# Performance work log

Hardware: AMD Instinct MI355X
Metric: run time of the kernel (lower is better)

## Reference

```python
import jax, jax.numpy as jnp
import numpy as np

ROWS, COLS = 1024, 1024
N_NODES = ROWS * COLS
RHO_W = 1000.0      # water density
RHO_I = 917.0       # ice density (unused in output path, kept for fidelity)
GRAV = 9.81
SEC_PER_A = 31556926.0
FLOW_COEFF = 0.0405
FLOW_EXP = 1.25     # 5/4
N_ITERS = 32        # fixed-point iterations for MFD flow accumulation


def _raster_links(rows, cols):
    ids = np.arange(rows * cols, dtype=np.int32).reshape(rows, cols)
    src_h = ids[:, :-1].ravel(); dst_h = ids[:, 1:].ravel()
    src_v = ids[:-1, :].ravel(); dst_v = ids[1:, :].ravel()
    return (np.concatenate([src_h, src_v]), np.concatenate([dst_h, dst_v]))


def setup_inputs() -> dict:
    key = jax.random.key(0)
    k1, k2, k3, k4 = jax.random.split(key, 4)
    melt_rate = jax.random.uniform(k1, (N_NODES,), jnp.float32) * 10.0          # m/a
    bedrock_elevation = jax.random.normal(k2, (N_NODES,), jnp.float32) * 500.0  # m
    water_pressure = jax.random.uniform(k3, (N_NODES,), jnp.float32) * 1.0e6    # Pa
    cell_area = jnp.full((N_NODES,), 1.0e4, jnp.float32)                        # 100m cells
    conduit_size = jax.random.uniform(k4, (N_NODES,), jnp.float32) + 0.01
    # landlab-style status: 0 = core node, 1 = fixed-value boundary (perimeter)
    status = np.zeros((ROWS, COLS), dtype=np.int32)
    status[0, :] = 1; status[-1, :] = 1; status[:, 0] = 1; status[:, -1] = 1
    src, dst = _raster_links(ROWS, COLS)
    return {
        "melt_rate": melt_rate,
        "bedrock_elevation": bedrock_elevation,
        "water_pressure": water_pressure,
        "cell_area": cell_area,
        "conduit_size": conduit_size,
        "status_at_node": jnp.asarray(status.ravel()),
        "link_src": jnp.asarray(src),
        "link_dst": jnp.asarray(dst),
    }


def reference(melt_rate, bedrock_elevation, water_pressure, cell_area,
              conduit_size, status_at_node, link_src, link_dst):
    n = melt_rate.shape[0]
    seg = lambda d, i: jax.ops.segment_sum(d, i, num_segments=n)

    # hydraulic potential (surface FlowDirectorMFD routes on)
    phi = RHO_W * GRAV * bedrock_elevation + water_pressure
    # local runoff input at each node
    runoff = melt_rate * cell_area / SEC_PER_A

    # MFD: split each node's outflow among downslope neighbors, proportional
    # to the positive potential drop along each link (unit link length).
    core = (status_at_node == 0)
    dphi = phi[link_src] - phi[link_dst]
    drop_fwd = jnp.maximum(dphi, 0.0) * core[link_src]   # src -> dst
    drop_bwd = jnp.maximum(-dphi, 0.0) * core[link_dst]  # dst -> src
    total_drop = seg(drop_fwd, link_src) + seg(drop_bwd, link_dst)
    s_safe = jnp.where(total_drop > 0.0, total_drop, 1.0)
    frac_fwd = drop_fwd / s_safe[link_src]
    frac_bwd = drop_bwd / s_safe[link_dst]

    # flow accumulation on the drainage DAG: Q = runoff + P^T Q (fixed-point)
    def step(q, _):
        inflow = seg(frac_fwd * q[link_src], link_dst) + seg(frac_bwd * q[link_dst], link_src)
        return runoff + inflow, None

    discharge, _ = jax.lax.scan(step, runoff, None, length=N_ITERS)

    # calc_hydraulic_gradient, masked to core nodes (status == 0)
    gradient = (discharge * FLOW_COEFF * conduit_size ** FLOW_EXP) ** 2
    return jnp.where(status_at_node == 0, gradient, 0.0)
```

## Files before the change

kernel.cpp:

```cpp
#include <hip/hip_runtime.h>

#define ROWS 1024
#define COLS 1024
#define NN (ROWS*COLS)

#define TILE_H 32
#define TILE_W 64
#define HALO   8
#define RH     48
#define RW     80
#define RC     (RH*RW)
#define SPR    (RW/4)
#define NSTRIP (RC/4)
#define NT     256
#define BR     (RH/4)
#define BC     (RW/4)
#define NB4    (BR*BC)

static constexpr float RHOG    = 1000.0f * 9.81f;
static constexpr float INV_SEC = 1.0f / 31556926.0f;
static constexpr float FLOWC   = 0.0405f;

__device__ __forceinline__ float4 gld4(const float* __restrict__ p, int g, bool in) {
    if (in) return *reinterpret_cast<const float4*>(p + g);
    return make_float4(0.f, 0.f, 0.f, 0.f);
}

__global__ __launch_bounds__(256) void k_pre(
        const float* __restrict__ bed, const float* __restrict__ pw,
        const int* __restrict__ status,
        const float* __restrict__ melt, const float* __restrict__ area,
        float* __restrict__ phi, float* __restrict__ inv,
        float* __restrict__ runoff) {
    int i = blockIdx.x * 256 + threadIdx.x;
    int r = i >> 10, c = i & (COLS - 1);
    float p = RHOG * bed[i] + pw[i];
    float t = 0.f;
    if (c > 0)        t += fmaxf(p - (RHOG * bed[i - 1]    + pw[i - 1]),    0.f);
    if (c < COLS - 1) t += fmaxf(p - (RHOG * bed[i + 1]    + pw[i + 1]),    0.f);
    if (r > 0)        t += fmaxf(p - (RHOG * bed[i - COLS] + pw[i - COLS]), 0.f);
    if (r < ROWS - 1) t += fmaxf(p - (RHOG * bed[i + COLS] + pw[i + COLS]), 0.f);
    phi[i]    = p;
    inv[i]    = (status[i] == 0 && t > 0.f) ? (1.f / t) : 0.f;
    runoff[i] = melt[i] * area[i] * INV_SEC;
}

template <bool FIRST, bool FINAL>
__global__ __launch_bounds__(256) void k_fused(
        const float* __restrict__ phi_g, const float* __restrict__ inv_g,
        const float* __restrict__ run_g, const float* __restrict__ qin,
        float* __restrict__ qout,
        const float* __restrict__ cond, const int* __restrict__ status) {
    __shared__ float A[RC];
    __shared__ float Bv[RC];
    __shared__ float4 plT[2][NB4], plB[2][NB4];
    __shared__ float4 plL[2][NB4], plR[2][NB4];
    const int tid = threadIdx.x;
    const int r0 = (int)blockIdx.y * TILE_H - HALO;
    const int c0 = (int)blockIdx.x * TILE_W - HALO;

#pragma unroll
    for (int k = 0; k < 4; ++k) {
        int sidx = tid + k * NT;
        if (sidx < NSTRIP) {
            int sr = sidx / SPR, sc4 = (sidx - sr * SPR) * 4;
            int gr = r0 + sr, gc = c0 + sc4;
            bool in = (gr >= 0) & (gr < ROWS) & (gc >= 0) & (gc < COLS);
            int g = gr * COLS + gc;
            *reinterpret_cast<float4*>(&A[sr * RW + sc4])  = gld4(phi_g, g, in);
            *reinterpret_cast<float4*>(&Bv[sr * RW + sc4]) = gld4(inv_g, g, in);
        }
    }
    __syncthreads();

    const bool active = (tid < NB4);
    const int br = tid / BC, bc = tid - (tid / BC) * BC;
    const int rr0 = 4 * br, cc0 = 4 * bc;
    const bool inter = (br >= 2) & (br <= BR - 3) & (bc >= 2) & (bc <= BC - 3);

    float wW[4][4], wE[4][4], wN[4][4], wS[4][4];
    float q[4][4], ro[4][4];
    int dd[4][4];

    if (active) {
#pragma unroll
        for (int i = 0; i < 4; ++i) {
            int rr = rr0 + i;
            int x = rr * RW + cc0;
            float4 pc = *reinterpret_cast<const float4*>(&A[x]);
            float4 ic = *reinterpret_cast<const float4*>(&Bv[x]);
            int xu = (rr > 0)      ? x - RW : x;
            int xd = (rr < RH - 1) ? x + RW : x;
            float4 pu = *reinterpret_cast<const float4*>(&A[xu]);
            float4 iu = *reinterpret_cast<const float4*>(&Bv[xu]);
            float4 pd = *reinterpret_cast<const float4*>(&A[xd]);
            float4 id = *reinterpret_cast<const float4*>(&Bv[xd]);
            float pl = (cc0 > 0)      ? A[x - 1]  : pc.x;
            float il = (cc0 > 0)      ? Bv[x - 1] : 0.f;
            float pr = (cc0 < RW - 4) ? A[x + 4]  : pc.w;
            float ir = (cc0 < RW - 4) ? Bv[x + 4] : 0.f;
            wN[i][0] = fmaxf(pu.x - pc.x, 0.f) * iu.x;
            wN[i][1] = fmaxf(pu.y - pc.y, 0.f) * iu.y;
            wN[i][2] = fmaxf(pu.z - pc.z, 0.f) * iu.z;
            wN[i][3] = fmaxf(pu.w - pc.w, 0.f) * iu.w;
            wS[i][0] = fmaxf(pd.x - pc.x, 0.f) * id.x;
            wS[i][1] = fmaxf(pd.y - pc.y, 0.f) * id.y;
            wS[i][2] = fmaxf(pd.z - pc.z, 0.f) * id.z;
            wS[i][3] = fmaxf(pd.w - pc.w, 0.f) * id.w;
            wW[i][0] = fmaxf(pl   - pc.x, 0.f) * il;
            wW[i][1] = fmaxf(pc.x - pc.y, 0.f) * ic.x;
            wW[i][2] = fmaxf(pc.y - pc.z, 0.f) * ic.y;
            wW[i][3] = fmaxf(pc.z - pc.w, 0.f) * ic.z;
            wE[i][0] = fmaxf(pc.y - pc.x, 0.f) * ic.y;
            wE[i][1] = fmaxf(pc.z - pc.y, 0.f) * ic.z;
            wE[i][2] = fmaxf(pc.w - pc.z, 0.f) * ic.w;
            wE[i][3] = fmaxf(pr   - pc.w, 0.f) * ir;
        }
#pragma unroll
        for (int i = 0; i < 4; ++i)
#pragma unroll
            for (int j = 0; j < 4; ++j) {
                int rr = rr0 + i, cc = cc0 + j;
                dd[i][j] = min(min(rr, RH - 1 - rr), min(cc, RW - 1 - cc));
            }
#pragma unroll
        for (int i = 0; i < 4; ++i) {
            int gr = r0 + rr0 + i, gc = c0 + cc0;
            bool in = (gr >= 0) & (gr < ROWS) & (gc >= 0) & (gc < COLS);
            int g = gr * COLS + gc;
            float4 r4 = gld4(run_g, g, in);
            ro[i][0] = r4.x; ro[i][1] = r4.y; ro[i][2] = r4.z; ro[i][3] = r4.w;
            float4 q4 = FIRST ? r4 : gld4(qin, g, in);
            q[i][0] = q4.x; q[i][1] = q4.y; q[i][2] = q4.z; q[i][3] = q4.w;
        }
        plT[0][tid] = make_float4(q[0][0], q[0][1], q[0][2], q[0][3]);
        plB[0][tid] = make_float4(q[3][0], q[3][1], q[3][2], q[3][3]);
        plL[0][tid] = make_float4(q[0][0], q[1][0], q[2][0], q[3][0]);
        plR[0][tid] = make_float4(q[0][3], q[1][3], q[2][3], q[3][3]);
    }
    __syncthreads();

    for (int s = 0; s < HALO; ++s) {
        const int pp = s & 1, pn = pp ^ 1;
        if (active) {
            float4 up = plB[pp][(br > 0)      ? tid - BC : tid];
            float4 dn = plT[pp][(br < BR - 1) ? tid + BC : tid];
            float4 lf = plR[pp][(bc > 0)      ? tid - 1  : tid];
            float4 rt = plL[pp][(bc < BC - 1) ? tid + 1  : tid];
            float upv[4] = {up.x, up.y, up.z, up.w};
            float dnv[4] = {dn.x, dn.y, dn.z, dn.w};
            float lfv[4] = {lf.x, lf.y, lf.z, lf.w};
            float rtv[4] = {rt.x, rt.y, rt.z, rt.w};
            float nq[4][4];
#pragma unroll
            for (int i = 0; i < 4; ++i)
#pragma unroll
                for (int j = 0; j < 4; ++j) {
                    float uv = (i > 0) ? q[i - 1][j] : upv[j];
                    float dv = (i < 3) ? q[i + 1][j] : dnv[j];
                    float lv = (j > 0) ? q[i][j - 1] : lfv[i];
                    float rv = (j < 3) ? q[i][j + 1] : rtv[i];
                    float a = ro[i][j];
                    a = fmaf(wW[i][j], lv, a);
                    a = fmaf(wE[i][j], rv, a);
                    a = fmaf(wN[i][j], uv, a);
                    a = fmaf(wS[i][j], dv, a);
                    nq[i][j] = a;
                }
            if (!inter) {
#pragma unroll
                for (int i = 0; i < 4; ++i)
#pragma unroll
                    for (int j = 0; j < 4; ++j)
                        nq[i][j] = (s < dd[i][j]) ? nq[i][j] : q[i][j];
            }
#pragma unroll
            for (int i = 0; i < 4; ++i)
#pragma unroll
                for (int j = 0; j < 4; ++j) q[i][j] = nq[i][j];
            plT[pn][tid] = make_float4(q[0][0], q[0][1], q[0][2], q[0][3]);
            plB[pn][tid] = make_float4(q[3][0], q[3][1], q[3][2], q[3][3]);
            plL[pn][tid] = make_float4(q[0][0], q[1][0], q[2][0], q[3][0]);
            plR[pn][tid] = make_float4(q[0][3], q[1][3], q[2][3], q[3][3]);
        }
        __syncthreads();
    }

    if (active && inter) {
#pragma unroll
        for (int i = 0; i < 4; ++i) {
            int g = (r0 + rr0 + i) * COLS + (c0 + cc0);
            if (FINAL) {
                float4 c4 = *reinterpret_cast<const float4*>(cond + g);
                int4 st   = *reinterpret_cast<const int4*>(status + g);
                float4 o;
                float t;
                t = q[i][0] * FLOWC * (c4.x * sqrtf(sqrtf(c4.x))); o.x = (st.x == 0) ? t * t : 0.f;
                t = q[i][1] * FLOWC * (c4.y * sqrtf(sqrtf(c4.y))); o.y = (st.y == 0) ? t * t : 0.f;
                t = q[i][2] * FLOWC * (c4.z * sqrtf(sqrtf(c4.z))); o.z = (st.z == 0) ? t * t : 0.f;
                t = q[i][3] * FLOWC * (c4.w * sqrtf(sqrtf(c4.w))); o.w = (st.w == 0) ? t * t : 0.f;
                *reinterpret_cast<float4*>(qout + g) = o;
            } else {
                *reinterpret_cast<float4*>(qout + g) =
                    make_float4(q[i][0], q[i][1], q[i][2], q[i][3]);
            }
        }
    }
}

extern "C" void kernel_launch(void* const* d_in, const int* in_sizes, int n_in,
                              void* d_out, int out_size, void* d_ws, size_t ws_size,
                              hipStream_t stream) {
    const float* melt   = (const float*)d_in[0];
    const float* bed    = (const float*)d_in[1];
    const float* pw     = (const float*)d_in[2];
    const float* area   = (const float*)d_in[3];
    const float* cond   = (const float*)d_in[4];
    const int*   status = (const int*)d_in[5];
    float* out = (float*)d_out;

    char* ws = (char*)d_ws;
    float* phi    = (float*)(ws);
    float* inv    = (float*)(ws + 4ull  * NN);
    float* runoff = (float*)(ws + 8ull  * NN);
    float* qA     = (float*)(ws + 12ull * NN);
    float* qB     = (float*)(ws + 16ull * NN);

    k_pre<<<dim3(NN / 256), dim3(256), 0, stream>>>(bed, pw, status, melt, area,
                                                    phi, inv, runoff);

    dim3 grid(COLS / TILE_W, ROWS / TILE_H), block(NT);
    k_fused<true,  false><<<grid, block, 0, stream>>>(phi, inv, runoff, runoff, qA, nullptr, nullptr);
    k_fused<false, false><<<grid, block, 0, stream>>>(phi, inv, runoff, qA, qB, nullptr, nullptr);
    k_fused<false, false><<<grid, block, 0, stream>>>(phi, inv, runoff, qB, qA, nullptr, nullptr);
    k_fused<false, true ><<<grid, block, 0, stream>>>(phi, inv, runoff, qA, out, cond, status);
}
```

Baseline: 141.8 us.

## Fuse preprocessing into stencil kernel and double halo to halve launches

Removes the separate preprocessing kernel: each tile now recomputes phi, the inverse total drop and runoff from raw inputs in shared memory, including a one-cell apron. The halo grows from 8 to 16, so 32 iterations take two fused launches instead of four, and the workspace arrays for phi, inv and runoff go away. In exchange each tile does more redundant halo work (a 64x96 region for a 32x64 output) with 384 threads, and the ping-pong planes reuse the phi LDS buffer after a barrier.

```diff
diff --git a/kernel.cpp b/kernel.cpp
--- a/kernel.cpp
+++ b/kernel.cpp
@@ -6,16 +6,21 @@
 
 #define TILE_H 32
 #define TILE_W 64
-#define HALO   8
-#define RH     48
-#define RW     80
+#define HALO   16
+#define RH     64
+#define RW     96
 #define RC     (RH*RW)
-#define SPR    (RW/4)
-#define NSTRIP (RC/4)
-#define NT     256
+#define NT     384
 #define BR     (RH/4)
 #define BC     (RW/4)
 #define NB4    (BR*BC)
+#define RSPR   (RW/4)
+
+#define APH    66
+#define APW    104
+#define APC    (APH*APW)
+#define APS    (APC/4)
+#define SPR    (APW/4)
 
 static constexpr float RHOG    = 1000.0f * 9.81f;
 static constexpr float INV_SEC = 1.0f / 31556926.0f;
@@ -25,168 +30,194 @@
     if (in) return *reinterpret_cast<const float4*>(p + g);
     return make_float4(0.f, 0.f, 0.f, 0.f);
 }
-
-__global__ __launch_bounds__(256) void k_pre(
-        const float* __restrict__ bed, const float* __restrict__ pw,
-        const int* __restrict__ status,
+__device__ __forceinline__ int4 gldi4(const int* __restrict__ p, int g, bool in) {
+    if (in) return *reinterpret_cast<const int4*>(p + g);
+    return make_int4(1, 1, 1, 1);
+}
+
+#define PLN(b,kind) (PL + (((b) * 4 + (kind)) * NB4))
+
+template <bool FIRST, bool FINAL>
+__global__ __launch_bounds__(NT, 3) void k_fused(
+        const float* __restrict__ bed,  const float* __restrict__ pw,
         const float* __restrict__ melt, const float* __restrict__ area,
-        float* __restrict__ phi, float* __restrict__ inv,
-        float* __restrict__ runoff) {
-    int i = blockIdx.x * 256 + threadIdx.x;
-    int r = i >> 10, c = i & (COLS - 1);
-    float p = RHOG * bed[i] + pw[i];
-    float t = 0.f;
-    if (c > 0)        t += fmaxf(p - (RHOG * bed[i - 1]    + pw[i - 1]),    0.f);
-    if (c < COLS - 1) t += fmaxf(p - (RHOG * bed[i + 1]    + pw[i + 1]),    0.f);
-    if (r > 0)        t += fmaxf(p - (RHOG * bed[i - COLS] + pw[i - COLS]), 0.f);
-    if (r < ROWS - 1) t += fmaxf(p - (RHOG * bed[i + COLS] + pw[i + COLS]), 0.f);
-    phi[i]    = p;
-    inv[i]    = (status[i] == 0 && t > 0.f) ? (1.f / t) : 0.f;
-    runoff[i] = melt[i] * area[i] * INV_SEC;
-}
-
-template <bool FIRST, bool FINAL>
-__global__ __launch_bounds__(256) void k_fused(
-        const float* __restrict__ phi_g, const float* __restrict__ inv_g,
-        const float* __restrict__ run_g, const float* __restrict__ qin,
-        float* __restrict__ qout,
+        const float* __restrict__ qin,  float* __restrict__ qout,
         const float* __restrict__ cond, const int* __restrict__ status) {
-    __shared__ float A[RC];
-    __shared__ float Bv[RC];
-    __shared__ float4 plT[2][NB4], plB[2][NB4];
-    __shared__ float4 plL[2][NB4], plR[2][NB4];
+    __shared__ __align__(16) float lds[APC + RC];
+    float*  AP = lds;
+    float*  Bv = lds + APC;
+    float4* PL = reinterpret_cast<float4*>(lds);
+
     const int tid = threadIdx.x;
     const int r0 = (int)blockIdx.y * TILE_H - HALO;
     const int c0 = (int)blockIdx.x * TILE_W - HALO;
 
 #pragma unroll
+    for (int k = 0; k < 5; ++k) {
+        int sidx = tid + k * NT;
+        if (sidx < APS) {
+            int sr = sidx / SPR, sc4 = (sidx - sr * SPR) * 4;
+            int gr = r0 - 1 + sr, gc = c0 - 4 + sc4;
+            bool in = (gr >= 0) & (gr < ROWS) & (gc >= 0) & (gc < COLS);
+            int g = gr * COLS + gc;
+            float4 b4 = gld4(bed, g, in);
+            float4 p4 = gld4(pw,  g, in);
+            float4 ph;
+            ph.x = fmaf(RHOG, b4.x, p4.x);
+            ph.y = fmaf(RHOG, b4.y, p4.y);
+            ph.z = fmaf(RHOG, b4.z, p4.z);
+            ph.w = fmaf(RHOG, b4.w, p4.w);
+            *reinterpret_cast<float4*>(&AP[sr * APW + sc4]) = ph;
+        }
+    }
+    __syncthreads();
+
+#pragma unroll
     for (int k = 0; k < 4; ++k) {
         int sidx = tid + k * NT;
-        if (sidx < NSTRIP) {
-            int sr = sidx / SPR, sc4 = (sidx - sr * SPR) * 4;
-            int gr = r0 + sr, gc = c0 + sc4;
-            bool in = (gr >= 0) & (gr < ROWS) & (gc >= 0) & (gc < COLS);
-            int g = gr * COLS + gc;
-            *reinterpret_cast<float4*>(&A[sr * RW + sc4])  = gld4(phi_g, g, in);
-            *reinterpret_cast<float4*>(&Bv[sr * RW + sc4]) = gld4(inv_g, g, in);
-        }
-    }
-    __syncthreads();
-
-    const bool active = (tid < NB4);
+        int sr = sidx / RSPR, sc4 = (sidx - sr * RSPR) * 4;
+        int x = (sr + 1) * APW + sc4 + 4;
+        float4 pc = *reinterpret_cast<const float4*>(&AP[x]);
+        float4 pu = *reinterpret_cast<const float4*>(&AP[x - APW]);
+        float4 pd = *reinterpret_cast<const float4*>(&AP[x + APW]);
+        float pl = AP[x - 1], pr = AP[x + 4];
+        float t0 = ((fmaxf(pc.x - pl,   0.f) + fmaxf(pc.x - pc.y, 0.f))
+                  +  fmaxf(pc.x - pu.x, 0.f)) + fmaxf(pc.x - pd.x, 0.f);
+        float t1 = ((fmaxf(pc.y - pc.x, 0.f) + fmaxf(pc.y - pc.z, 0.f))
+                  +  fmaxf(pc.y - pu.y, 0.f)) + fmaxf(pc.y - pd.y, 0.f);
+        float t2 = ((fmaxf(pc.z - pc.y, 0.f) + fmaxf(pc.z - pc.w, 0.f))
+                  +  fmaxf(pc.z - pu.z, 0.f)) + fmaxf(pc.z - pd.z, 0.f);
+        float t3 = ((fmaxf(pc.w - pc.z, 0.f) + fmaxf(pc.w - pr,   0.f))
+                  +  fmaxf(pc.w - pu.w, 0.f)) + fmaxf(pc.w - pd.w, 0.f);
+        int gr = r0 + sr, gc = c0 + sc4;
+        bool in = (gr >= 0) & (gr < ROWS) & (gc >= 0) & (gc < COLS);
+        int4 st = gldi4(status, gr * COLS + gc, in);
+        float4 iv;
+        iv.x = (st.x == 0 && t0 > 0.f) ? 1.f / t0 : 0.f;
+        iv.y = (st.y == 0 && t1 > 0.f) ? 1.f / t1 : 0.f;
+        iv.z = (st.z == 0 && t2 > 0.f) ? 1.f / t2 : 0.f;
+        iv.w = (st.w == 0 && t3 > 0.f) ? 1.f / t3 : 0.f;
+        *reinterpret_cast<float4*>(&Bv[sr * RW + sc4]) = iv;
+    }
+    __syncthreads();
+
     const int br = tid / BC, bc = tid - (tid / BC) * BC;
     const int rr0 = 4 * br, cc0 = 4 * bc;
-    const bool inter = (br >= 2) & (br <= BR - 3) & (bc >= 2) & (bc <= BC - 3);
+    const bool inter = (br >= 4) & (br <= BR - 5) & (bc >= 4) & (bc <= BC - 5);
 
     float wW[4][4], wE[4][4], wN[4][4], wS[4][4];
     float q[4][4], ro[4][4];
-    int dd[4][4];
-
-    if (active) {
-#pragma unroll
-        for (int i = 0; i < 4; ++i) {
-            int rr = rr0 + i;
-            int x = rr * RW + cc0;
-            float4 pc = *reinterpret_cast<const float4*>(&A[x]);
-            float4 ic = *reinterpret_cast<const float4*>(&Bv[x]);
-            int xu = (rr > 0)      ? x - RW : x;
-            int xd = (rr < RH - 1) ? x + RW : x;
-            float4 pu = *reinterpret_cast<const float4*>(&A[xu]);
-            float4 iu = *reinterpret_cast<const float4*>(&Bv[xu]);
-            float4 pd = *reinterpret_cast<const float4*>(&A[xd]);
-            float4 id = *reinterpret_cast<const float4*>(&Bv[xd]);
-            float pl = (cc0 > 0)      ? A[x - 1]  : pc.x;
-            float il = (cc0 > 0)      ? Bv[x - 1] : 0.f;
-            float pr = (cc0 < RW - 4) ? A[x + 4]  : pc.w;
-            float ir = (cc0 < RW - 4) ? Bv[x + 4] : 0.f;
-            wN[i][0] = fmaxf(pu.x - pc.x, 0.f) * iu.x;
-            wN[i][1] = fmaxf(pu.y - pc.y, 0.f) * iu.y;
-            wN[i][2] = fmaxf(pu.z - pc.z, 0.f) * iu.z;
-            wN[i][3] = fmaxf(pu.w - pc.w, 0.f) * iu.w;
-            wS[i][0] = fmaxf(pd.x - pc.x, 0.f) * id.x;
-            wS[i][1] = fmaxf(pd.y - pc.y, 0.f) * id.y;
-            wS[i][2] = fmaxf(pd.z - pc.z, 0.f) * id.z;
-            wS[i][3] = fmaxf(pd.w - pc.w, 0.f) * id.w;
-            wW[i][0] = fmaxf(pl   - pc.x, 0.f) * il;
-            wW[i][1] = fmaxf(pc.x - pc.y, 0.f) * ic.x;
-            wW[i][2] = fmaxf(pc.y - pc.z, 0.f) * ic.y;
-            wW[i][3] = fmaxf(pc.z - pc.w, 0.f) * ic.z;
-            wE[i][0] = fmaxf(pc.y - pc.x, 0.f) * ic.y;
-            wE[i][1] = fmaxf(pc.z - pc.y, 0.f) * ic.z;
-            wE[i][2] = fmaxf(pc.w - pc.z, 0.f) * ic.w;
-            wE[i][3] = fmaxf(pr   - pc.w, 0.f) * ir;
-        }
-#pragma unroll
-        for (int i = 0; i < 4; ++i)
-#pragma unroll
-            for (int j = 0; j < 4; ++j) {
-                int rr = rr0 + i, cc = cc0 + j;
-                dd[i][j] = min(min(rr, RH - 1 - rr), min(cc, RW - 1 - cc));
-            }
-#pragma unroll
-        for (int i = 0; i < 4; ++i) {
-            int gr = r0 + rr0 + i, gc = c0 + cc0;
-            bool in = (gr >= 0) & (gr < ROWS) & (gc >= 0) & (gc < COLS);
-            int g = gr * COLS + gc;
-            float4 r4 = gld4(run_g, g, in);
-            ro[i][0] = r4.x; ro[i][1] = r4.y; ro[i][2] = r4.z; ro[i][3] = r4.w;
-            float4 q4 = FIRST ? r4 : gld4(qin, g, in);
+    int dr_[4], dc_[4];
+
+#pragma unroll
+    for (int i = 0; i < 4; ++i) {
+        int rr = rr0 + i;
+        int xp = (rr + 1) * APW + cc0 + 4;
+        float4 pc = *reinterpret_cast<const float4*>(&AP[xp]);
+        float4 pu = *reinterpret_cast<const float4*>(&AP[xp - APW]);
+        float4 pd = *reinterpret_cast<const float4*>(&AP[xp + APW]);
+        float pl = AP[xp - 1], pr = AP[xp + 4];
+        int xb = rr * RW + cc0;
+        float4 ic = *reinterpret_cast<const float4*>(&Bv[xb]);
+        float4 iu = *reinterpret_cast<const float4*>(&Bv[(rr > 0)      ? xb - RW : xb]);
+        float4 id = *reinterpret_cast<const float4*>(&Bv[(rr < RH - 1) ? xb + RW : xb]);
+        float il = (cc0 > 0)      ? Bv[xb - 1] : 0.f;
+        float ir = (cc0 < RW - 4) ? Bv[xb + 4] : 0.f;
+        wN[i][0] = fmaxf(pu.x - pc.x, 0.f) * iu.x;
+        wN[i][1] = fmaxf(pu.y - pc.y, 0.f) * iu.y;
+        wN[i][2] = fmaxf(pu.z - pc.z, 0.f) * iu.z;
+        wN[i][3] = fmaxf(pu.w - pc.w, 0.f) * iu.w;
+        wS[i][0] = fmaxf(pd.x - pc.x, 0.f) * id.x;
+        wS[i][1] = fmaxf(pd.y - pc.y, 0.f) * id.y;
+        wS[i][2] = fmaxf(pd.z - pc.z, 0.f) * id.z;
+        wS[i][3] = fmaxf(pd.w - pc.w, 0.f) * id.w;
+        wW[i][0] = fmaxf(pl   - pc.x, 0.f) * il;
+        wW[i][1] = fmaxf(pc.x - pc.y, 0.f) * ic.x;
+        wW[i][2] = fmaxf(pc.y - pc.z, 0.f) * ic.y;
+        wW[i][3] = fmaxf(pc.z - pc.w, 0.f) * ic.z;
+        wE[i][0] = fmaxf(pc.y - pc.x, 0.f) * ic.y;
+        wE[i][1] = fmaxf(pc.z - pc.y, 0.f) * ic.z;
+        wE[i][2] = fmaxf(pc.w - pc.z, 0.f) * ic.w;
+        wE[i][3] = fmaxf(pr   - pc.w, 0.f) * ir;
+    }
+#pragma unroll
+    for (int i = 0; i < 4; ++i) {
+        int rr = rr0 + i, cc = cc0 + i;
+        dr_[i] = min(rr, RH - 1 - rr);
+        dc_[i] = min(cc, RW - 1 - cc);
+    }
+#pragma unroll
+    for (int i = 0; i < 4; ++i) {
+        int gr = r0 + rr0 + i, gc = c0 + cc0;
+        bool in = (gr >= 0) & (gr < ROWS) & (gc >= 0) & (gc < COLS);
+        int g = gr * COLS + gc;
+        float4 m4 = gld4(melt, g, in);
+        float4 a4 = gld4(area, g, in);
+        ro[i][0] = m4.x * a4.x * INV_SEC;
+        ro[i][1] = m4.y * a4.y * INV_SEC;
+        ro[i][2] = m4.z * a4.z * INV_SEC;
+        ro[i][3] = m4.w * a4.w * INV_SEC;
+        if (FIRST) {
+            q[i][0] = ro[i][0]; q[i][1] = ro[i][1];
+            q[i][2] = ro[i][2]; q[i][3] = ro[i][3];
+        } else {
+            float4 q4 = gld4(qin, g, in);
             q[i][0] = q4.x; q[i][1] = q4.y; q[i][2] = q4.z; q[i][3] = q4.w;
         }
-        plT[0][tid] = make_float4(q[0][0], q[0][1], q[0][2], q[0][3]);
-        plB[0][tid] = make_float4(q[3][0], q[3][1], q[3][2], q[3][3]);
-        plL[0][tid] = make_float4(q[0][0], q[1][0], q[2][0], q[3][0]);
-        plR[0][tid] = make_float4(q[0][3], q[1][3], q[2][3], q[3][3]);
-    }
+    }
+    __syncthreads();
+
+    PLN(0,0)[tid] = make_float4(q[0][0], q[0][1], q[0][2], q[0][3]);
+    PLN(0,1)[tid] = make_float4(q[3][0], q[3][1], q[3][2], q[3][3]);
+    PLN(0,2)[tid] = make_float4(q[0][0], q[1][0], q[2][0], q[3][0]);
+    PLN(0,3)[tid] = make_float4(q[0][3], q[1][3], q[2][3], q[3][3]);
     __syncthreads();
 
     for (int s = 0; s < HALO; ++s) {
         const int pp = s & 1, pn = pp ^ 1;
-        if (active) {
-            float4 up = plB[pp][(br > 0)      ? tid - BC : tid];
-            float4 dn = plT[pp][(br < BR - 1) ? tid + BC : tid];
-            float4 lf = plR[pp][(bc > 0)      ? tid - 1  : tid];
-            float4 rt = plL[pp][(bc < BC - 1) ? tid + 1  : tid];
-            float upv[4] = {up.x, up.y, up.z, up.w};
-            float dnv[4] = {dn.x, dn.y, dn.z, dn.w};
-            float lfv[4] = {lf.x, lf.y, lf.z, lf.w};
-            float rtv[4] = {rt.x, rt.y, rt.z, rt.w};
-            float nq[4][4];
+        float4 up = PLN(pp,1)[(br > 0)      ? tid - BC : tid];
+        float4 dn = PLN(pp,0)[(br < BR - 1) ? tid + BC : tid];
+        float4 lf = PLN(pp,3)[(bc > 0)      ? tid - 1  : tid];
+        float4 rt = PLN(pp,2)[(bc < BC - 1) ? tid + 1  : tid];
+        float upv[4] = {up.x, up.y, up.z, up.w};
+        float dnv[4] = {dn.x, dn.y, dn.z, dn.w};
+        float lfv[4] = {lf.x, lf.y, lf.z, lf.w};
+        float rtv[4] = {rt.x, rt.y, rt.z, rt.w};
+        float nq[4][4];
+#pragma unroll
+        for (int i = 0; i < 4; ++i)
+#pragma unroll
+            for (int j = 0; j < 4; ++j) {
+                float uv = (i > 0) ? q[i - 1][j] : upv[j];
+                float dv = (i < 3) ? q[i + 1][j] : dnv[j];
+                float lv = (j > 0) ? q[i][j - 1] : lfv[i];
+                float rv = (j < 3) ? q[i][j + 1] : rtv[i];
+                float a = ro[i][j];
+                a = fmaf(wW[i][j], lv, a);
+                a = fmaf(wE[i][j], rv, a);
+                a = fmaf(wN[i][j], uv, a);
+                a = fmaf(wS[i][j], dv, a);
+                nq[i][j] = a;
+            }
+        if (!inter) {
 #pragma unroll
             for (int i = 0; i < 4; ++i)
 #pragma unroll
-                for (int j = 0; j < 4; ++j) {
-                    float uv = (i > 0) ? q[i - 1][j] : upv[j];
-                    float dv = (i < 3) ? q[i + 1][j] : dnv[j];
-                    float lv = (j > 0) ? q[i][j - 1] : lfv[i];
-                    float rv = (j < 3) ? q[i][j + 1] : rtv[i];
-                    float a = ro[i][j];
-                    a = fmaf(wW[i][j], lv, a);
-                    a = fmaf(wE[i][j], rv, a);
-                    a = fmaf(wN[i][j], uv, a);
-                    a = fmaf(wS[i][j], dv, a);
-                    nq[i][j] = a;
-                }
-            if (!inter) {
-#pragma unroll
-                for (int i = 0; i < 4; ++i)
-#pragma unroll
-                    for (int j = 0; j < 4; ++j)
-                        nq[i][j] = (s < dd[i][j]) ? nq[i][j] : q[i][j];
-            }
-#pragma unroll
-            for (int i = 0; i < 4; ++i)
-#pragma unroll
-                for (int j = 0; j < 4; ++j) q[i][j] = nq[i][j];
-            plT[pn][tid] = make_float4(q[0][0], q[0][1], q[0][2], q[0][3]);
-            plB[pn][tid] = make_float4(q[3][0], q[3][1], q[3][2], q[3][3]);
-            plL[pn][tid] = make_float4(q[0][0], q[1][0], q[2][0], q[3][0]);
-            plR[pn][tid] = make_float4(q[0][3], q[1][3], q[2][3], q[3][3]);
-        }
+                for (int j = 0; j < 4; ++j)
+                    nq[i][j] = (s < min(dr_[i], dc_[j])) ? nq[i][j] : q[i][j];
+        }
+#pragma unroll
+        for (int i = 0; i < 4; ++i)
+#pragma unroll
+            for (int j = 0; j < 4; ++j) q[i][j] = nq[i][j];
+        PLN(pn,0)[tid] = make_float4(q[0][0], q[0][1], q[0][2], q[0][3]);
+        PLN(pn,1)[tid] = make_float4(q[3][0], q[3][1], q[3][2], q[3][3]);
+        PLN(pn,2)[tid] = make_float4(q[0][0], q[1][0], q[2][0], q[3][0]);
+        PLN(pn,3)[tid] = make_float4(q[0][3], q[1][3], q[2][3], q[3][3]);
         __syncthreads();
     }
 
-    if (active && inter) {
+    if (inter) {
 #pragma unroll
         for (int i = 0; i < 4; ++i) {
             int g = (r0 + rr0 + i) * COLS + (c0 + cc0);
@@ -218,20 +249,9 @@
     const float* cond   = (const float*)d_in[4];
     const int*   status = (const int*)d_in[5];
     float* out = (float*)d_out;
-
-    char* ws = (char*)d_ws;
-    float* phi    = (float*)(ws);
-    float* inv    = (float*)(ws + 4ull  * NN);
-    float* runoff = (float*)(ws + 8ull  * NN);
-    float* qA     = (float*)(ws + 12ull * NN);
-    float* qB     = (float*)(ws + 16ull * NN);
-
-    k_pre<<<dim3(NN / 256), dim3(256), 0, stream>>>(bed, pw, status, melt, area,
-                                                    phi, inv, runoff);
+    float* qA  = (float*)d_ws;
 
     dim3 grid(COLS / TILE_W, ROWS / TILE_H), block(NT);
-    k_fused<true,  false><<<grid, block, 0, stream>>>(phi, inv, runoff, runoff, qA, nullptr, nullptr);
-    k_fused<false, false><<<grid, block, 0, stream>>>(phi, inv, runoff, qA, qB, nullptr, nullptr);
-    k_fused<false, false><<<grid, block, 0, stream>>>(phi, inv, runoff, qB, qA, nullptr, nullptr);
-    k_fused<false, true ><<<grid, block, 0, stream>>>(phi, inv, runoff, qA, out, cond, status);
-}
+    k_fused<true,  false><<<grid, block, 0, stream>>>(bed, pw, melt, area, nullptr, qA, nullptr, status);
+    k_fused<false, true ><<<grid, block, 0, stream>>>(bed, pw, melt, area, qA, out, cond, status);
+}
```

New measurement: 157.4 us. +11.0%, slower.

## Use 2x4 micro-tiles with 512 threads and alias plane buffers onto tile LDS

Applied to the files above, without the earlier changes.

Each thread now owns a 2x4 micro-tile instead of 4x4, and the block grows to 512 threads with launch bounds asking for two blocks per SM. This cuts register use per thread and raises parallelism. The left/right plane exchange shrinks to float2, and the ping-pong planes reuse the LDS that held the phi/inv tile once the weights are computed, which costs an extra barrier. The per-cell distance mask for halo freezing is removed, and runoff/q loads are issued before the LDS fill.

```diff
diff --git a/kernel.cpp b/kernel.cpp
--- a/kernel.cpp
+++ b/kernel.cpp
@@ -10,12 +10,12 @@
 #define RH     48
 #define RW     80
 #define RC     (RH*RW)
+#define NT     512
+#define BR     (RH/2)
+#define BC     (RW/4)
+#define NB     (BR*BC)
+#define NSTRIP (RC/4)
 #define SPR    (RW/4)
-#define NSTRIP (RC/4)
-#define NT     256
-#define BR     (RH/4)
-#define BC     (RW/4)
-#define NB4    (BR*BC)
 
 static constexpr float RHOG    = 1000.0f * 9.81f;
 static constexpr float INV_SEC = 1.0f / 31556926.0f;
@@ -45,22 +45,48 @@
     runoff[i] = melt[i] * area[i] * INV_SEC;
 }
 
+#define LDSF   11520
+
 template <bool FIRST, bool FINAL>
-__global__ __launch_bounds__(256) void k_fused(
+__global__ __launch_bounds__(NT, 2) void k_fused(
         const float* __restrict__ phi_g, const float* __restrict__ inv_g,
         const float* __restrict__ run_g, const float* __restrict__ qin,
         float* __restrict__ qout,
         const float* __restrict__ cond, const int* __restrict__ status) {
-    __shared__ float A[RC];
-    __shared__ float Bv[RC];
-    __shared__ float4 plT[2][NB4], plB[2][NB4];
-    __shared__ float4 plL[2][NB4], plR[2][NB4];
+    __shared__ __align__(16) float lds[LDSF];
+    float*  A  = lds;
+    float*  Bv = lds + RC;
+    float4* pT = reinterpret_cast<float4*>(lds);
+    float4* pB = reinterpret_cast<float4*>(lds) + 2 * NB;
+    float2* pL = reinterpret_cast<float2*>(lds + 7680);
+    float2* pR = reinterpret_cast<float2*>(lds + 9600);
+
     const int tid = threadIdx.x;
     const int r0 = (int)blockIdx.y * TILE_H - HALO;
     const int c0 = (int)blockIdx.x * TILE_W - HALO;
 
-#pragma unroll
-    for (int k = 0; k < 4; ++k) {
+    const bool active = (tid < NB);
+    const int br = tid / BC, bc = tid - (tid / BC) * BC;
+    const int rr0 = 2 * br, cc0 = 4 * bc;
+    const bool inter = (br >= 4) & (br <= BR - 5) & (bc >= 2) & (bc <= BC - 3);
+
+    float q[2][4], ro[2][4];
+
+    if (active) {
+#pragma unroll
+        for (int i = 0; i < 2; ++i) {
+            int gr = r0 + rr0 + i, gc = c0 + cc0;
+            bool in = (gr >= 0) & (gr < ROWS) & (gc >= 0) & (gc < COLS);
+            int g = gr * COLS + gc;
+            float4 r4 = gld4(run_g, g, in);
+            ro[i][0] = r4.x; ro[i][1] = r4.y; ro[i][2] = r4.z; ro[i][3] = r4.w;
+            float4 q4 = FIRST ? r4 : gld4(qin, g, in);
+            q[i][0] = q4.x; q[i][1] = q4.y; q[i][2] = q4.z; q[i][3] = q4.w;
+        }
+    }
+
+#pragma unroll
+    for (int k = 0; k < 2; ++k) {
         int sidx = tid + k * NT;
         if (sidx < NSTRIP) {
             int sr = sidx / SPR, sc4 = (sidx - sr * SPR) * 4;
@@ -73,18 +99,10 @@
     }
     __syncthreads();
 
-    const bool active = (tid < NB4);
-    const int br = tid / BC, bc = tid - (tid / BC) * BC;
-    const int rr0 = 4 * br, cc0 = 4 * bc;
-    const bool inter = (br >= 2) & (br <= BR - 3) & (bc >= 2) & (bc <= BC - 3);
-
-    float wW[4][4], wE[4][4], wN[4][4], wS[4][4];
-    float q[4][4], ro[4][4];
-    int dd[4][4];
-
+    float wW[2][4], wE[2][4], wN[2][4], wS[2][4];
     if (active) {
 #pragma unroll
-        for (int i = 0; i < 4; ++i) {
+        for (int i = 0; i < 2; ++i) {
             int rr = rr0 + i;
             int x = rr * RW + cc0;
             float4 pc = *reinterpret_cast<const float4*>(&A[x]);
@@ -116,48 +134,35 @@
             wE[i][2] = fmaxf(pc.w - pc.z, 0.f) * ic.w;
             wE[i][3] = fmaxf(pr   - pc.w, 0.f) * ir;
         }
-#pragma unroll
-        for (int i = 0; i < 4; ++i)
-#pragma unroll
-            for (int j = 0; j < 4; ++j) {
-                int rr = rr0 + i, cc = cc0 + j;
-                dd[i][j] = min(min(rr, RH - 1 - rr), min(cc, RW - 1 - cc));
-            }
-#pragma unroll
-        for (int i = 0; i < 4; ++i) {
-            int gr = r0 + rr0 + i, gc = c0 + cc0;
-            bool in = (gr >= 0) & (gr < ROWS) & (gc >= 0) & (gc < COLS);
-            int g = gr * COLS + gc;
-            float4 r4 = gld4(run_g, g, in);
-            ro[i][0] = r4.x; ro[i][1] = r4.y; ro[i][2] = r4.z; ro[i][3] = r4.w;
-            float4 q4 = FIRST ? r4 : gld4(qin, g, in);
-            q[i][0] = q4.x; q[i][1] = q4.y; q[i][2] = q4.z; q[i][3] = q4.w;
-        }
-        plT[0][tid] = make_float4(q[0][0], q[0][1], q[0][2], q[0][3]);
-        plB[0][tid] = make_float4(q[3][0], q[3][1], q[3][2], q[3][3]);
-        plL[0][tid] = make_float4(q[0][0], q[1][0], q[2][0], q[3][0]);
-        plR[0][tid] = make_float4(q[0][3], q[1][3], q[2][3], q[3][3]);
+    }
+    __syncthreads();
+
+    if (active) {
+        pT[tid]          = make_float4(q[0][0], q[0][1], q[0][2], q[0][3]);
+        pB[tid]          = make_float4(q[1][0], q[1][1], q[1][2], q[1][3]);
+        pL[tid]          = make_float2(q[0][0], q[1][0]);
+        pR[tid]          = make_float2(q[0][3], q[1][3]);
     }
     __syncthreads();
 
     for (int s = 0; s < HALO; ++s) {
         const int pp = s & 1, pn = pp ^ 1;
         if (active) {
-            float4 up = plB[pp][(br > 0)      ? tid - BC : tid];
-            float4 dn = plT[pp][(br < BR - 1) ? tid + BC : tid];
-            float4 lf = plR[pp][(bc > 0)      ? tid - 1  : tid];
-            float4 rt = plL[pp][(bc < BC - 1) ? tid + 1  : tid];
+            float4 up = pB[pp * NB + ((br > 0)      ? tid - BC : tid)];
+            float4 dn = pT[pp * NB + ((br < BR - 1) ? tid + BC : tid)];
+            float2 lf = pR[pp * NB + ((bc > 0)      ? tid - 1  : tid)];
+            float2 rt = pL[pp * NB + ((bc < BC - 1) ? tid + 1  : tid)];
             float upv[4] = {up.x, up.y, up.z, up.w};
             float dnv[4] = {dn.x, dn.y, dn.z, dn.w};
-            float lfv[4] = {lf.x, lf.y, lf.z, lf.w};
-            float rtv[4] = {rt.x, rt.y, rt.z, rt.w};
-            float nq[4][4];
-#pragma unroll
-            for (int i = 0; i < 4; ++i)
+            float lfv[2] = {lf.x, lf.y};
+            float rtv[2] = {rt.x, rt.y};
+            float nq[2][4];
+#pragma unroll
+            for (int i = 0; i < 2; ++i)
 #pragma unroll
                 for (int j = 0; j < 4; ++j) {
-                    float uv = (i > 0) ? q[i - 1][j] : upv[j];
-                    float dv = (i < 3) ? q[i + 1][j] : dnv[j];
+                    float uv = (i > 0) ? q[0][j] : upv[j];
+                    float dv = (i < 1) ? q[1][j] : dnv[j];
                     float lv = (j > 0) ? q[i][j - 1] : lfv[i];
                     float rv = (j < 3) ? q[i][j + 1] : rtv[i];
                     float a = ro[i][j];
@@ -167,28 +172,21 @@
                     a = fmaf(wS[i][j], dv, a);
                     nq[i][j] = a;
                 }
-            if (!inter) {
-#pragma unroll
-                for (int i = 0; i < 4; ++i)
-#pragma unroll
-                    for (int j = 0; j < 4; ++j)
-                        nq[i][j] = (s < dd[i][j]) ? nq[i][j] : q[i][j];
-            }
-#pragma unroll
-            for (int i = 0; i < 4; ++i)
+#pragma unroll
+            for (int i = 0; i < 2; ++i)
 #pragma unroll
                 for (int j = 0; j < 4; ++j) q[i][j] = nq[i][j];
-            plT[pn][tid] = make_float4(q[0][0], q[0][1], q[0][2], q[0][3]);
-            plB[pn][tid] = make_float4(q[3][0], q[3][1], q[3][2], q[3][3]);
-            plL[pn][tid] = make_float4(q[0][0], q[1][0], q[2][0], q[3][0]);
-            plR[pn][tid] = make_float4(q[0][3], q[1][3], q[2][3], q[3][3]);
+            pT[pn * NB + tid] = make_float4(q[0][0], q[0][1], q[0][2], q[0][3]);
+            pB[pn * NB + tid] = make_float4(q[1][0], q[1][1], q[1][2], q[1][3]);
+            pL[pn * NB + tid] = make_float2(q[0][0], q[1][0]);
+            pR[pn * NB + tid] = make_float2(q[0][3], q[1][3]);
         }
         __syncthreads();
     }
 
     if (active && inter) {
 #pragma unroll
-        for (int i = 0; i < 4; ++i) {
+        for (int i = 0; i < 2; ++i) {
             int g = (r0 + rr0 + i) * COLS + (c0 + cc0);
             if (FINAL) {
                 float4 c4 = *reinterpret_cast<const float4*>(cond + g);
```

Measured after the change: 144.2 us. About the same (+1.7%).

## Replace shared-memory block tiles with per-wavefront register tiles using shuffles

Applied to the files above, without the earlier changes.

Each 64-lane wavefront now owns a 32x32 region (16x16 output plus an 8-cell halo), with each lane holding a 4x4 sub-tile in registers. Neighbor exchange for phi, inv and q goes through wavefront shuffles instead of shared memory plus __syncthreads, which removes LDS staging and block-level barriers. In exchange, halo redundancy grows from 48x80 per 32x64 output to 32x32 per 16x16 output, so global loads and recomputation per output cell roughly double. The per-cell distance mask is also dropped, so halo cells near the region edge now update with clamped neighbor values, though only interior outputs are written.

```diff
diff --git a/kernel.cpp b/kernel.cpp
--- a/kernel.cpp
+++ b/kernel.cpp
@@ -4,18 +4,14 @@
 #define COLS 1024
 #define NN (ROWS*COLS)
 
-#define TILE_H 32
-#define TILE_W 64
-#define HALO   8
-#define RH     48
-#define RW     80
-#define RC     (RH*RW)
-#define SPR    (RW/4)
-#define NSTRIP (RC/4)
-#define NT     256
-#define BR     (RH/4)
-#define BC     (RW/4)
-#define NB4    (BR*BC)
+#define OT    16
+#define HALO  8
+#define RS    32
+#define TPD   (COLS/OT)
+#define NWAVE (TPD*TPD)
+#define WPB   4
+#define NT    (WPB*64)
+#define NBLK  (NWAVE/WPB)
 
 static constexpr float RHOG    = 1000.0f * 9.81f;
 static constexpr float INV_SEC = 1.0f / 31556926.0f;
@@ -46,162 +42,138 @@
 }
 
 template <bool FIRST, bool FINAL>
-__global__ __launch_bounds__(256) void k_fused(
+__global__ __launch_bounds__(NT, 3) void k_step(
         const float* __restrict__ phi_g, const float* __restrict__ inv_g,
         const float* __restrict__ run_g, const float* __restrict__ qin,
         float* __restrict__ qout,
         const float* __restrict__ cond, const int* __restrict__ status) {
-    __shared__ float A[RC];
-    __shared__ float Bv[RC];
-    __shared__ float4 plT[2][NB4], plB[2][NB4];
-    __shared__ float4 plL[2][NB4], plR[2][NB4];
-    const int tid = threadIdx.x;
-    const int r0 = (int)blockIdx.y * TILE_H - HALO;
-    const int c0 = (int)blockIdx.x * TILE_W - HALO;
-
-#pragma unroll
-    for (int k = 0; k < 4; ++k) {
-        int sidx = tid + k * NT;
-        if (sidx < NSTRIP) {
-            int sr = sidx / SPR, sc4 = (sidx - sr * SPR) * 4;
-            int gr = r0 + sr, gc = c0 + sc4;
-            bool in = (gr >= 0) & (gr < ROWS) & (gc >= 0) & (gc < COLS);
-            int g = gr * COLS + gc;
-            *reinterpret_cast<float4*>(&A[sr * RW + sc4])  = gld4(phi_g, g, in);
-            *reinterpret_cast<float4*>(&Bv[sr * RW + sc4]) = gld4(inv_g, g, in);
-        }
-    }
-    __syncthreads();
-
-    const bool active = (tid < NB4);
-    const int br = tid / BC, bc = tid - (tid / BC) * BC;
-    const int rr0 = 4 * br, cc0 = 4 * bc;
-    const bool inter = (br >= 2) & (br <= BR - 3) & (bc >= 2) & (bc <= BC - 3);
+    const int tid  = threadIdx.x;
+    const int lane = tid & 63;
+    const int wid  = blockIdx.x * WPB + (tid >> 6);
+    const int tr = wid >> 6, tc = wid & (TPD - 1);
+    const int R0 = tr * OT - HALO, C0 = tc * OT - HALO;
+    const int wr = lane >> 3, wc = lane & 7;
+    const int gr0 = R0 + wr * 4, gc0 = C0 + wc * 4;
+
+    const int upL = (wr > 0) ? lane - 8 : lane;
+    const int dnL = (wr < 7) ? lane + 8 : lane;
+    const int lfL = (wc > 0) ? lane - 1 : lane;
+    const int rtL = (wc < 7) ? lane + 1 : lane;
+
+    const bool cin = ((unsigned)gc0 < COLS);
+    bool in[4];
+    int  g[4];
+#pragma unroll
+    for (int i = 0; i < 4; ++i) {
+        in[i] = ((unsigned)(gr0 + i) < ROWS) & cin;
+        g[i]  = (gr0 + i) * COLS + gc0;
+    }
+
+    float ph[4][4], iv[4][4];
+#pragma unroll
+    for (int i = 0; i < 4; ++i) {
+        float4 p4 = gld4(phi_g, g[i], in[i]);
+        float4 i4 = gld4(inv_g, g[i], in[i]);
+        ph[i][0]=p4.x; ph[i][1]=p4.y; ph[i][2]=p4.z; ph[i][3]=p4.w;
+        iv[i][0]=i4.x; iv[i][1]=i4.y; iv[i][2]=i4.z; iv[i][3]=i4.w;
+    }
+
+    float phU[4], phD[4], ivU[4], ivD[4], phL[4], phR[4], ivL[4], ivR[4];
+#pragma unroll
+    for (int j = 0; j < 4; ++j) {
+        phU[j] = __shfl(ph[3][j], upL, 64);  ivU[j] = __shfl(iv[3][j], upL, 64);
+        phD[j] = __shfl(ph[0][j], dnL, 64);  ivD[j] = __shfl(iv[0][j], dnL, 64);
+    }
+#pragma unroll
+    for (int i = 0; i < 4; ++i) {
+        phL[i] = __shfl(ph[i][3], lfL, 64);  ivL[i] = __shfl(iv[i][3], lfL, 64);
+        phR[i] = __shfl(ph[i][0], rtL, 64);  ivR[i] = __shfl(iv[i][0], rtL, 64);
+    }
 
     float wW[4][4], wE[4][4], wN[4][4], wS[4][4];
+#pragma unroll
+    for (int i = 0; i < 4; ++i)
+#pragma unroll
+        for (int j = 0; j < 4; ++j) {
+            float pc = ph[i][j];
+            float pu = (i > 0) ? ph[i-1][j] : phU[j];
+            float iu = (i > 0) ? iv[i-1][j] : ivU[j];
+            float pd = (i < 3) ? ph[i+1][j] : phD[j];
+            float id = (i < 3) ? iv[i+1][j] : ivD[j];
+            float pl = (j > 0) ? ph[i][j-1] : phL[i];
+            float il = (j > 0) ? iv[i][j-1] : ivL[i];
+            float pr = (j < 3) ? ph[i][j+1] : phR[i];
+            float ir = (j < 3) ? iv[i][j+1] : ivR[i];
+            wN[i][j] = fmaxf(pu - pc, 0.f) * iu;
+            wS[i][j] = fmaxf(pd - pc, 0.f) * id;
+            wW[i][j] = fmaxf(pl - pc, 0.f) * il;
+            wE[i][j] = fmaxf(pr - pc, 0.f) * ir;
+        }
+
     float q[4][4], ro[4][4];
-    int dd[4][4];
-
-    if (active) {
+#pragma unroll
+    for (int i = 0; i < 4; ++i) {
+        float4 r4 = gld4(run_g, g[i], in[i]);
+        ro[i][0]=r4.x; ro[i][1]=r4.y; ro[i][2]=r4.z; ro[i][3]=r4.w;
+        if (FIRST) {
+            q[i][0]=r4.x; q[i][1]=r4.y; q[i][2]=r4.z; q[i][3]=r4.w;
+        } else {
+            float4 q4 = gld4(qin, g[i], in[i]);
+            q[i][0]=q4.x; q[i][1]=q4.y; q[i][2]=q4.z; q[i][3]=q4.w;
+        }
+    }
+
+#pragma unroll
+    for (int s = 0; s < HALO; ++s) {
+        float u[4], d[4], l[4], r[4];
+#pragma unroll
+        for (int j = 0; j < 4; ++j) {
+            u[j] = __shfl(q[3][j], upL, 64);
+            d[j] = __shfl(q[0][j], dnL, 64);
+        }
 #pragma unroll
         for (int i = 0; i < 4; ++i) {
-            int rr = rr0 + i;
-            int x = rr * RW + cc0;
-            float4 pc = *reinterpret_cast<const float4*>(&A[x]);
-            float4 ic = *reinterpret_cast<const float4*>(&Bv[x]);
-            int xu = (rr > 0)      ? x - RW : x;
-            int xd = (rr < RH - 1) ? x + RW : x;
-            float4 pu = *reinterpret_cast<const float4*>(&A[xu]);
-            float4 iu = *reinterpret_cast<const float4*>(&Bv[xu]);
-            float4 pd = *reinterpret_cast<const float4*>(&A[xd]);
-            float4 id = *reinterpret_cast<const float4*>(&Bv[xd]);
-            float pl = (cc0 > 0)      ? A[x - 1]  : pc.x;
-            float il = (cc0 > 0)      ? Bv[x - 1] : 0.f;
-            float pr = (cc0 < RW - 4) ? A[x + 4]  : pc.w;
-            float ir = (cc0 < RW - 4) ? Bv[x + 4] : 0.f;
-            wN[i][0] = fmaxf(pu.x - pc.x, 0.f) * iu.x;
-            wN[i][1] = fmaxf(pu.y - pc.y, 0.f) * iu.y;
-            wN[i][2] = fmaxf(pu.z - pc.z, 0.f) * iu.z;
-            wN[i][3] = fmaxf(pu.w - pc.w, 0.f) * iu.w;
-            wS[i][0] = fmaxf(pd.x - pc.x, 0.f) * id.x;
-            wS[i][1] = fmaxf(pd.y - pc.y, 0.f) * id.y;
-            wS[i][2] = fmaxf(pd.z - pc.z, 0.f) * id.z;
-            wS[i][3] = fmaxf(pd.w - pc.w, 0.f) * id.w;
-            wW[i][0] = fmaxf(pl   - pc.x, 0.f) * il;
-            wW[i][1] = fmaxf(pc.x - pc.y, 0.f) * ic.x;
-            wW[i][2] = fmaxf(pc.y - pc.z, 0.f) * ic.y;
-            wW[i][3] = fmaxf(pc.z - pc.w, 0.f) * ic.z;
-            wE[i][0] = fmaxf(pc.y - pc.x, 0.f) * ic.y;
-            wE[i][1] = fmaxf(pc.z - pc.y, 0.f) * ic.z;
-            wE[i][2] = fmaxf(pc.w - pc.z, 0.f) * ic.w;
-            wE[i][3] = fmaxf(pr   - pc.w, 0.f) * ir;
-        }
+            l[i] = __shfl(q[i][3], lfL, 64);
+            r[i] = __shfl(q[i][0], rtL, 64);
+        }
+        float nq[4][4];
 #pragma unroll
         for (int i = 0; i < 4; ++i)
 #pragma unroll
             for (int j = 0; j < 4; ++j) {
-                int rr = rr0 + i, cc = cc0 + j;
-                dd[i][j] = min(min(rr, RH - 1 - rr), min(cc, RW - 1 - cc));
+                float uv = (i > 0) ? q[i-1][j] : u[j];
+                float dv = (i < 3) ? q[i+1][j] : d[j];
+                float lv = (j > 0) ? q[i][j-1] : l[i];
+                float rv = (j < 3) ? q[i][j+1] : r[i];
+                float a = ro[i][j];
+                a = fmaf(wW[i][j], lv, a);
+                a = fmaf(wE[i][j], rv, a);
+                a = fmaf(wN[i][j], uv, a);
+                a = fmaf(wS[i][j], dv, a);
+                nq[i][j] = a;
             }
 #pragma unroll
+        for (int i = 0; i < 4; ++i)
+#pragma unroll
+            for (int j = 0; j < 4; ++j) q[i][j] = nq[i][j];
+    }
+
+    if ((wr >= 2) & (wr < 6) & (wc >= 2) & (wc < 6)) {
+#pragma unroll
         for (int i = 0; i < 4; ++i) {
-            int gr = r0 + rr0 + i, gc = c0 + cc0;
-            bool in = (gr >= 0) & (gr < ROWS) & (gc >= 0) & (gc < COLS);
-            int g = gr * COLS + gc;
-            float4 r4 = gld4(run_g, g, in);
-            ro[i][0] = r4.x; ro[i][1] = r4.y; ro[i][2] = r4.z; ro[i][3] = r4.w;
-            float4 q4 = FIRST ? r4 : gld4(qin, g, in);
-            q[i][0] = q4.x; q[i][1] = q4.y; q[i][2] = q4.z; q[i][3] = q4.w;
-        }
-        plT[0][tid] = make_float4(q[0][0], q[0][1], q[0][2], q[0][3]);
-        plB[0][tid] = make_float4(q[3][0], q[3][1], q[3][2], q[3][3]);
-        plL[0][tid] = make_float4(q[0][0], q[1][0], q[2][0], q[3][0]);
-        plR[0][tid] = make_float4(q[0][3], q[1][3], q[2][3], q[3][3]);
-    }
-    __syncthreads();
-
-    for (int s = 0; s < HALO; ++s) {
-        const int pp = s & 1, pn = pp ^ 1;
-        if (active) {
-            float4 up = plB[pp][(br > 0)      ? tid - BC : tid];
-            float4 dn = plT[pp][(br < BR - 1) ? tid + BC : tid];
-            float4 lf = plR[pp][(bc > 0)      ? tid - 1  : tid];
-            float4 rt = plL[pp][(bc < BC - 1) ? tid + 1  : tid];
-            float upv[4] = {up.x, up.y, up.z, up.w};
-            float dnv[4] = {dn.x, dn.y, dn.z, dn.w};
-            float lfv[4] = {lf.x, lf.y, lf.z, lf.w};
-            float rtv[4] = {rt.x, rt.y, rt.z, rt.w};
-            float nq[4][4];
-#pragma unroll
-            for (int i = 0; i < 4; ++i)
-#pragma unroll
-                for (int j = 0; j < 4; ++j) {
-                    float uv = (i > 0) ? q[i - 1][j] : upv[j];
-                    float dv = (i < 3) ? q[i + 1][j] : dnv[j];
-                    float lv = (j > 0) ? q[i][j - 1] : lfv[i];
-                    float rv = (j < 3) ? q[i][j + 1] : rtv[i];
-                    float a = ro[i][j];
-                    a = fmaf(wW[i][j], lv, a);
-                    a = fmaf(wE[i][j], rv, a);
-                    a = fmaf(wN[i][j], uv, a);
-                    a = fmaf(wS[i][j], dv, a);
-                    nq[i][j] = a;
-                }
-            if (!inter) {
-#pragma unroll
-                for (int i = 0; i < 4; ++i)
-#pragma unroll
-                    for (int j = 0; j < 4; ++j)
-                        nq[i][j] = (s < dd[i][j]) ? nq[i][j] : q[i][j];
-            }
-#pragma unroll
-            for (int i = 0; i < 4; ++i)
-#pragma unroll
-                for (int j = 0; j < 4; ++j) q[i][j] = nq[i][j];
-            plT[pn][tid] = make_float4(q[0][0], q[0][1], q[0][2], q[0][3]);
-            plB[pn][tid] = make_float4(q[3][0], q[3][1], q[3][2], q[3][3]);
-            plL[pn][tid] = make_float4(q[0][0], q[1][0], q[2][0], q[3][0]);
-            plR[pn][tid] = make_float4(q[0][3], q[1][3], q[2][3], q[3][3]);
-        }
-        __syncthreads();
-    }
-
-    if (active && inter) {
-#pragma unroll
-        for (int i = 0; i < 4; ++i) {
-            int g = (r0 + rr0 + i) * COLS + (c0 + cc0);
+            int go = g[i];
             if (FINAL) {
-                float4 c4 = *reinterpret_cast<const float4*>(cond + g);
-                int4 st   = *reinterpret_cast<const int4*>(status + g);
+                float4 c4 = *reinterpret_cast<const float4*>(cond + go);
+                int4 st   = *reinterpret_cast<const int4*>(status + go);
                 float4 o;
                 float t;
                 t = q[i][0] * FLOWC * (c4.x * sqrtf(sqrtf(c4.x))); o.x = (st.x == 0) ? t * t : 0.f;
                 t = q[i][1] * FLOWC * (c4.y * sqrtf(sqrtf(c4.y))); o.y = (st.y == 0) ? t * t : 0.f;
                 t = q[i][2] * FLOWC * (c4.z * sqrtf(sqrtf(c4.z))); o.z = (st.z == 0) ? t * t : 0.f;
                 t = q[i][3] * FLOWC * (c4.w * sqrtf(sqrtf(c4.w))); o.w = (st.w == 0) ? t * t : 0.f;
-                *reinterpret_cast<float4*>(qout + g) = o;
+                *reinterpret_cast<float4*>(qout + go) = o;
             } else {
-                *reinterpret_cast<float4*>(qout + g) =
+                *reinterpret_cast<float4*>(qout + go) =
                     make_float4(q[i][0], q[i][1], q[i][2], q[i][3]);
             }
         }
@@ -229,9 +201,9 @@
     k_pre<<<dim3(NN / 256), dim3(256), 0, stream>>>(bed, pw, status, melt, area,
                                                     phi, inv, runoff);
 
-    dim3 grid(COLS / TILE_W, ROWS / TILE_H), block(NT);
-    k_fused<true,  false><<<grid, block, 0, stream>>>(phi, inv, runoff, runoff, qA, nullptr, nullptr);
-    k_fused<false, false><<<grid, block, 0, stream>>>(phi, inv, runoff, qA, qB, nullptr, nullptr);
-    k_fused<false, false><<<grid, block, 0, stream>>>(phi, inv, runoff, qB, qA, nullptr, nullptr);
-    k_fused<false, true ><<<grid, block, 0, stream>>>(phi, inv, runoff, qA, out, cond, status);
-}
+    dim3 grid(NBLK), block(NT);
+    k_step<true,  false><<<grid, block, 0, stream>>>(phi, inv, runoff, runoff, qA, nullptr, nullptr);
+    k_step<false, false><<<grid, block, 0, stream>>>(phi, inv, runoff, qA, qB, nullptr, nullptr);
+    k_step<false, false><<<grid, block, 0, stream>>>(phi, inv, runoff, qB, qA, nullptr, nullptr);
+    k_step<false, true ><<<grid, block, 0, stream>>>(phi, inv, runoff, qA, out, cond, status);
+}
```

New measurement: 271.9 us. 1.92x slower.
